# Kernel tuning notes

Measured on AMD Instinct MI355X. Metric: run time of the kernel, lower is better.

## Reference

```python
import jax, jax.numpy as jnp
import numpy as np
from math import factorial

# ---- static config (mirrors init_kwargs) ----
ZS = np.array([1, 6, 7, 8], dtype=np.int64)
NZ = 4
N_ATOM_BASIS = 3
CHAN = N_ATOM_BASIS ** 2          # 9 edge channels
MAX_L = 3
N_RBF = 8                          # radial basis functions
N_RB = 8                           # radial embedding dim
CUTOFF = 5.5
P_CUT = 6
MP_NORM = 1.0 / 10.0 ** 0.5        # 1/sqrt(avg_num_neighbors)
NUM_MP = 1
N_NODES = 4000
N_EDGES = 48000

def _make_l_list(max_l):
    lst = []
    for l in range(max_l + 1):
        for lx in range(l, -1, -1):
            for ly in range(l - lx, -1, -1):
                lst.append((lx, ly, l - lx - ly))
    return lst

L_LIST = _make_l_list(MAX_L)       # 20 (lx,ly,lz) tuples
N_L = len(L_LIST)
L_OF = np.array([sum(t) for t in L_LIST], dtype=np.int32)
LX = np.array([t[0] for t in L_LIST])
LY = np.array([t[1] for t in L_LIST])
LZ = np.array([t[2] for t in L_LIST])
# multinomial prefactors l!/(lx!ly!lz!), grouped per l for the nu=2 symmetrizer
PREF = np.array([factorial(sum(t)) / (factorial(t[0]) * factorial(t[1]) * factorial(t[2])) for t in L_LIST], dtype=np.float32)
SYM2 = np.zeros((N_L, MAX_L + 1), dtype=np.float32)
SYM2[np.arange(N_L), L_OF] = PREF

def _bessel_rbf(r):
    # r: [E,1] -> [E, N_RBF];  e_n(r) = sqrt(2/rc) * sin(n pi r / rc) / r
    n = jnp.arange(1, N_RBF + 1, dtype=r.dtype)
    return jnp.sqrt(2.0 / CUTOFF) * jnp.sin(n * jnp.pi * r / CUTOFF) / r

def _poly_cutoff(r):
    p = float(P_CUT)
    u = r / CUTOFF
    f = 1.0 - 0.5 * (p + 1.0) * (p + 2.0) * u ** p + p * (p + 2.0) * u ** (p + 1.0) - 0.5 * p * (p + 1.0) * u ** (p + 2.0)
    return f * (u < 1.0)

def _angular(unit):
    # monomials x^lx * y^ly * z^lz of the unit edge vector -> [E, N_L]
    x, y, z = unit[:, 0:1], unit[:, 1:2], unit[:, 2:3]
    return (x ** jnp.asarray(LX)) * (y ** jnp.asarray(LY)) * (z ** jnp.asarray(LZ))

def _radial_transform(A, W_rt):
    # shared per-l linear map along radial axis: [N, N_RBF, N_L, C] -> [N, N_RB, N_L, C]
    Wg = W_rt[jnp.asarray(L_OF)]   # [N_L, N_RBF, N_RB]
    return jnp.einsum('nric,irs->nsic', A, Wg)

def _symmetrize(A):
    # nu=1: A at lxlylz=(0,0,0); nu=2, each l: sum_{|lxlylz|=l} multinomial * A^2
    B1 = A[:, :, 0:1, :]
    B2 = jnp.einsum('nric,il->nrlc', A * A, jnp.asarray(SYM2))
    return jnp.concatenate([B1, B2], axis=2)   # [N, N_RB, 1+(MAX_L+1), C]

def _forward(positions, shifts, W_emb, W_rt, W_nm, atomic_numbers, edge_index):
    sender, receiver = edge_index[0], edge_index[1]
    one_hot = (atomic_numbers[:, None] == jnp.asarray(ZS)[None, :]).astype(positions.dtype)
    node_emb = one_hot @ W_emb                                    # [N, n_atom_basis]
    # edge encoding: flattened outer product of sender/receiver embeddings -> [E, CHAN]
    enc = (node_emb[sender][:, :, None] * node_emb[receiver][:, None, :]).reshape(-1, CHAN)
    vec = positions[receiver] - positions[sender] + shifts
    lengths = jnp.linalg.norm(vec, axis=-1, keepdims=True)        # [E,1]
    unit = vec / lengths
    rc = _bessel_rbf(lengths) * _poly_cutoff(lengths)             # [E, N_RBF]
    ang = _angular(unit)                                          # [E, N_L]
    edge_attri = rc[:, :, None, None] * ang[:, None, :, None] * enc[:, None, None, :]
    A = jax.ops.segment_sum(edge_attri, receiver, num_segments=N_NODES)
    A = _radial_transform(A, W_rt)                                # [N, N_RB, N_L, C]
    B = _symmetrize(A)
    feats = [B]
    Wnm_exp = W_nm[:, :, jnp.asarray(L_OF), :]                    # expand per-l memory weights to lxlylz
    for _ in range(NUM_MP):
        memory = A * Wnm_exp                                      # NodeMemory
        chi = B.sum(axis=(1, 2))                                  # [N, C] invariant scalar per channel
        msg_B = edge_attri * chi[sender][:, None, None, :]        # MesssageBchi
        A_B = _radial_transform(jax.ops.segment_sum(msg_B, receiver, num_segments=N_NODES), W_rt)
        msg_A = A[sender] * rc[:, :, None, None]                  # MessageAr: radial-weighted sender A
        A = (A_B + jax.ops.segment_sum(msg_A, receiver, num_segments=N_NODES)) * MP_NORM + memory
        B = _symmetrize(A)
        feats.append(B)
    return jnp.stack(feats, axis=-1)                              # [N, N_RB, 5, C, 1+NUM_MP]

def setup_inputs() -> dict:
    key = jax.random.key(0)
    k = jax.random.split(key, 8)
    positions = jax.random.uniform(k[0], (N_NODES, 3), dtype=jnp.float32) * 3.0
    shifts = jnp.zeros((N_EDGES, 3), dtype=jnp.float32)
    species_idx = jax.random.randint(k[1], (N_NODES,), 0, NZ)
    atomic_numbers = jnp.asarray(ZS)[species_idx]
    sender = jax.random.randint(k[2], (N_EDGES,), 0, N_NODES)
    receiver = (sender + 1 + jax.random.randint(k[3], (N_EDGES,), 0, N_NODES - 1)) % N_NODES  # no self-edges
    edge_index = jnp.stack([sender, receiver])
    W_emb = jax.random.normal(k[4], (NZ, N_ATOM_BASIS), dtype=jnp.float32) * 0.5
    W_rt = jax.random.normal(k[5], (MAX_L + 1, N_RBF, N_RB), dtype=jnp.float32) / np.sqrt(N_RBF)
    W_nm = jax.random.uniform(k[6], (1, N_RB, MAX_L + 1, CHAN), dtype=jnp.float32)
    return {"positions": positions, "shifts": shifts, "W_emb": W_emb, "W_rt": W_rt, "W_nm": W_nm, "atomic_numbers": atomic_numbers, "edge_index": edge_index}

def reference(positions, shifts, W_emb, W_rt, W_nm, atomic_numbers, edge_index):
    return _forward(positions, shifts, W_emb, W_rt, W_nm, atomic_numbers, edge_index)
```

## Files before the change

### kernel.cpp

```cpp
#include <hip/hip_runtime.h>
#include <hip/hip_fp16.h>

#ifndef M_PIf
#define M_PIf 3.14159265358979323846f
#endif

constexpr int NNODE = 4000;
constexpr int NEDGE = 48000;
constexpr int NLA   = 20;
constexpr int NCH   = 9;
constexpr int NRB   = 8;
constexpr int NEL   = NRB * NLA * NCH;
constexpr int NP2   = NEL / 2;
constexpr int FW    = 40;
constexpr int EC    = 32;
constexpr float CUT = 5.5f;
constexpr float MPN = 0.316227766016837933f;

__constant__ int   c_LOF[NLA]  = {0,1,1,1,2,2,2,2,2,2,3,3,3,3,3,3,3,3,3,3};
__constant__ float c_PREF[NLA] = {1,1,1,1,1,2,2,1,2,1,1,3,3,3,6,3,1,3,3,1};
__constant__ int   c_GB[4] = {0,0,1,4};
__constant__ int   c_GE[4] = {0,1,4,10};

__global__ void k_count(const int* __restrict__ ei, int* __restrict__ counts) {
  int e = blockIdx.x * blockDim.x + threadIdx.x;
  if (e >= NEDGE) return;
  atomicAdd(&counts[ei[NEDGE + e]], 1);
}

__global__ void k_scan(const int* __restrict__ counts, int* __restrict__ offsets,
                       int* __restrict__ cursor) {
  __shared__ int lds[1024];
  int t = threadIdx.x;
  int base = t*4;
  int c0 = (base+0 < NNODE) ? counts[base+0] : 0;
  int c1 = (base+1 < NNODE) ? counts[base+1] : 0;
  int c2 = (base+2 < NNODE) ? counts[base+2] : 0;
  int c3 = (base+3 < NNODE) ? counts[base+3] : 0;
  lds[t] = c0+c1+c2+c3;
  __syncthreads();
  for (int d = 1; d < 1024; d <<= 1) {
    int v = (t >= d) ? lds[t-d] : 0;
    __syncthreads();
    lds[t] += v;
    __syncthreads();
  }
  int excl = (t == 0) ? 0 : lds[t-1];
  int o0 = excl, o1 = o0+c0, o2 = o1+c1, o3 = o2+c2;
  if (base+0 < NNODE) { offsets[base+0]=o0; cursor[base+0]=o0; }
  if (base+1 < NNODE) { offsets[base+1]=o1; cursor[base+1]=o1; }
  if (base+2 < NNODE) { offsets[base+2]=o2; cursor[base+2]=o2; }
  if (base+3 < NNODE) { offsets[base+3]=o3; cursor[base+3]=o3; }
  if (t == 1023) offsets[NNODE] = lds[1023];
}

__global__ void k_edgec(const float* __restrict__ pos, const float* __restrict__ shifts,
                        const int* __restrict__ ei, const int* __restrict__ an,
                        const float* __restrict__ W_emb,
                        int* __restrict__ cursor, float* __restrict__ facS,
                        int* __restrict__ sndS) {
  int e = blockIdx.x * blockDim.x + threadIdx.x;
  if (e >= NEDGE) return;
  int snd = ei[e];
  int rcv = ei[NEDGE + e];
  float vx = pos[rcv*3+0] - pos[snd*3+0] + shifts[e*3+0];
  float vy = pos[rcv*3+1] - pos[snd*3+1] + shifts[e*3+1];
  float vz = pos[rcv*3+2] - pos[snd*3+2] + shifts[e*3+2];
  float len = sqrtf(vx*vx + vy*vy + vz*vz);
  float inv = 1.0f / len;
  float x = vx*inv, y = vy*inv, z = vz*inv;
  float u  = len * (1.0f/CUT);
  float u2 = u*u;
  float u6 = u2*u2*u2;
  float fcut = 1.0f - 28.0f*u6 + 48.0f*u6*u - 21.0f*u6*u2;
  if (u >= 1.0f) fcut = 0.0f;
  float pre = sqrtf(2.0f/CUT) * fcut * inv;
  int p = atomicAdd(&cursor[rcv], 1);
  float* f = facS + (size_t)p*FW;
  #pragma unroll
  for (int j = 0; j < NRB; ++j)
    f[j] = pre * sinf((float)(j+1) * M_PIf * u);
  float ang[NLA];
  ang[0]=1.0f; ang[1]=x; ang[2]=y; ang[3]=z;
  ang[4]=x*x; ang[5]=x*y; ang[6]=x*z; ang[7]=y*y; ang[8]=y*z; ang[9]=z*z;
  ang[10]=ang[4]*x; ang[11]=ang[4]*y; ang[12]=ang[4]*z;
  ang[13]=x*ang[7]; ang[14]=ang[5]*z; ang[15]=x*ang[9];
  ang[16]=ang[7]*y; ang[17]=ang[7]*z; ang[18]=y*ang[9]; ang[19]=ang[9]*z;
  #pragma unroll
  for (int i = 0; i < NLA; ++i) f[8+i] = ang[i];
  int as_ = an[snd], ar_ = an[rcv];
  int sps = (as_==1)?0:(as_==6)?1:(as_==7)?2:3;
  int spr = (ar_==1)?0:(ar_==6)?1:(ar_==7)?2:3;
  float es0=W_emb[sps*3+0], es1=W_emb[sps*3+1], es2=W_emb[sps*3+2];
  float er0=W_emb[spr*3+0], er1=W_emb[spr*3+1], er2=W_emb[spr*3+2];
  f[28]=es0*er0; f[29]=es0*er1; f[30]=es0*er2;
  f[31]=es1*er0; f[32]=es1*er1; f[33]=es1*er2;
  f[34]=es2*er0; f[35]=es2*er1; f[36]=es2*er2;
  f[37]=0.f; f[38]=0.f; f[39]=0.f;
  sndS[p] = snd;
}

__global__ void k_echi(const float* __restrict__ facS, const int* __restrict__ sndS,
                       const float* __restrict__ chi, float* __restrict__ echiS) {
  int p = blockIdx.x * blockDim.x + threadIdx.x;
  if (p >= NEDGE) return;
  int snd = sndS[p];
  const float* f = facS + (size_t)p*FW;
  float* o = echiS + (size_t)p*12;
  #pragma unroll
  for (int c = 0; c < 9; ++c)
    o[c] = chi[snd*9 + c] * f[28 + c];
  o[9] = 0.f; o[10] = 0.f; o[11] = 0.f;
}


__global__ __launch_bounds__(256, 8) void k_nodeA(
    const float* __restrict__ facS, const int* __restrict__ offsets,
    const float* __restrict__ W_rt,
    float2* __restrict__ A1f2, __half2* __restrict__ A1h2,
    float* __restrict__ chi, float* __restrict__ out) {
  __shared__ float s_wrt[256];
  __shared__ float s_e[EC*FW];
  __shared__ float s_tile[8*90];
  __shared__ float s_B[288];
  int bid = blockIdx.x;
  int n = bid >> 1, half = bid & 1;
  int t = threadIdx.x;
  s_wrt[t] = W_rt[t];
  int rq[2], kk[2], i0[2], c0[2], l0[2], i1[2], c1[2], l1[2], qg[2];
  bool val[2];
  #pragma unroll
  for (int jj = 0; jj < 2; ++jj) {
    int j = t + jj*256;
    val[jj] = (j < 360);
    int js = val[jj] ? j : 0;
    rq[jj] = js / 45; kk[jj] = js % 45;
    qg[jj] = rq[jj]*90 + kk[jj] + half*45;
    int rem0 = 2*(kk[jj] + 45*half);
    i0[jj] = rem0 / 9;  c0[jj] = rem0 % 9;  l0[jj] = c_LOF[i0[jj]];
    int rem1 = rem0 + 1;
    i1[jj] = rem1 / 9;  c1[jj] = rem1 % 9;  l1[jj] = c_LOF[i1[jj]];
  }
  float acc[2][2] = {{0,0},{0,0}};
  int beg = offsets[n], end = offsets[n+1];
  const float4* f4 = (const float4*)facS;
  for (int base = beg; base < end; base += EC) {
    int m = min(EC, end - base);
    __syncthreads();
    for (int idx = t; idx < m*(FW/4); idx += 256)
      ((float4*)s_e)[idx] = f4[(size_t)base*(FW/4) + idx];
    __syncthreads();
    for (int p = 0; p < m; ++p) {
      const float* e0 = s_e + p*FW;
      #pragma unroll
      for (int jj = 0; jj < 2; ++jj) {
        if (val[jj]) {
          float rv = e0[rq[jj]];
          acc[jj][0] += rv * e0[8+i0[jj]] * e0[28+c0[jj]];
          acc[jj][1] += rv * e0[8+i1[jj]] * e0[28+c1[jj]];
        }
      }
    }
  }
  __syncthreads();
  #pragma unroll
  for (int jj = 0; jj < 2; ++jj)
    if (val[jj]) {
      s_tile[rq[jj]*90 + 2*kk[jj]]     = acc[jj][0];
      s_tile[rq[jj]*90 + 2*kk[jj] + 1] = acc[jj][1];
    }
  __syncthreads();
  float a1v[2][2];
  #pragma unroll
  for (int jj = 0; jj < 2; ++jj) {
    if (val[jj]) {
      float ab0 = 0.f, ab1 = 0.f;
      #pragma unroll
      for (int r = 0; r < NRB; ++r) {
        ab0 += s_tile[r*90 + 2*kk[jj]]     * s_wrt[l0[jj]*64 + r*8 + rq[jj]];
        ab1 += s_tile[r*90 + 2*kk[jj] + 1] * s_wrt[l1[jj]*64 + r*8 + rq[jj]];
      }
      a1v[jj][0] = ab0; a1v[jj][1] = ab1;
      size_t qi = (size_t)n*NP2 + qg[jj];
      A1f2[qi] = make_float2(ab0, ab1);
      A1h2[qi] = __floats2half2_rn(ab0, ab1);
    }
  }
  __syncthreads();
  #pragma unroll
  for (int jj = 0; jj < 2; ++jj)
    if (val[jj]) {
      s_tile[rq[jj]*90 + 2*kk[jj]]     = a1v[jj][0];
      s_tile[rq[jj]*90 + 2*kk[jj] + 1] = a1v[jj][1];
    }
  __syncthreads();
  if (half == 0) {
    for (int m2 = t; m2 < 288; m2 += 256) {
      int s = m2 / 36, rm = m2 % 36, l5 = rm / 9, c = rm % 9;
      float b;
      if (l5 == 0) b = s_tile[s*90 + c];
      else {
        b = 0.f;
        for (int i = c_GB[l5]; i < c_GE[l5]; ++i) {
          float v = s_tile[s*90 + i*9 + c];
          b += c_PREF[i]*v*v;
        }
      }
      out[(size_t)(((n*8 + s)*5 + l5)*9 + c)*2 + 0] = b;
      s_B[m2] = b;
    }
    __syncthreads();
    if (t < 9) {
      float x = 0.f;
      #pragma unroll
      for (int u = 0; u < 32; ++u) x += s_B[u*9 + t];
      atomicAdd(&chi[n*9 + t], x);
    }
  } else {
    if (t < 72) {
      int s = t / 9, c = t % 9;
      float b = 0.f;
      for (int i = 10; i < 20; ++i) {
        float v = s_tile[s*90 + (i-10)*9 + c];
        b += c_PREF[i]*v*v;
      }
      out[(size_t)(((n*8 + s)*5 + 4)*9 + c)*2 + 0] = b;
      s_B[t] = b;
    }
    __syncthreads();
    if (t < 9) {
      float x = 0.f;
      #pragma unroll
      for (int u = 0; u < 8; ++u) x += s_B[u*9 + t];
      atomicAdd(&chi[n*9 + t], x);
    }
  }
}

__global__ __launch_bounds__(256, 8) void k_nodeMP(
    const float* __restrict__ facS, const int* __restrict__ offsets,
    const int* __restrict__ sndS, const float* __restrict__ echiS,
    const float* __restrict__ W_rt, const float* __restrict__ W_nm,
    const float2* __restrict__ A1f2, const __half2* __restrict__ A1h2,
    float* __restrict__ out) {
  __shared__ float s_wrt[256];
  __shared__ float s_wnm[288];
  __shared__ float s_e[EC*FW];
  __shared__ float s_ec[EC*12];
  __shared__ float s_tile[8*90];
  int bid = blockIdx.x;
  int n = bid >> 1, half = bid & 1;
  int t = threadIdx.x;
  s_wrt[t] = W_rt[t];
  s_wnm[t] = W_nm[t];
  if (t < 32) s_wnm[256 + t] = W_nm[256 + t];
  int rq[2], kk[2], i0[2], c0[2], l0[2], i1[2], c1[2], l1[2], qg[2];
  bool val[2];
  #pragma unroll
  for (int jj = 0; jj < 2; ++jj) {
    int j = t + jj*256;
    val[jj] = (j < 360);
    int js = val[jj] ? j : 0;
    rq[jj] = js / 45; kk[jj] = js % 45;
    qg[jj] = rq[jj]*90 + kk[jj] + half*45;
    int rem0 = 2*(kk[jj] + 45*half);
    i0[jj] = rem0 / 9;  c0[jj] = rem0 % 9;  l0[jj] = c_LOF[i0[jj]];
    int rem1 = rem0 + 1;
    i1[jj] = rem1 / 9;  c1[jj] = rem1 % 9;  l1[jj] = c_LOF[i1[jj]];
  }
  float accA[2][2] = {{0,0},{0,0}};
  float accB[2][2] = {{0,0},{0,0}};
  float2 mymem[2];
  #pragma unroll
  for (int jj = 0; jj < 2; ++jj)
    mymem[jj] = val[jj] ? A1f2[(size_t)n*NP2 + qg[jj]] : make_float2(0.f, 0.f);
  int beg = offsets[n], end = offsets[n+1];
  const float4* f4 = (const float4*)facS;
  const float4* e4 = (const float4*)echiS;
  for (int base = beg; base < end; base += EC) {
    int m = min(EC, end - base);
    __syncthreads();
    for (int idx = t; idx < m*(FW/4); idx += 256)
      ((float4*)s_e)[idx] = f4[(size_t)base*(FW/4) + idx];
    for (int idx = t; idx < m*3; idx += 256)
      ((float4*)s_ec)[idx] = e4[(size_t)base*3 + idx];
    __syncthreads();
    int p = 0;
    for (; p + 3 < m; p += 4) {
      int sd0 = sndS[base+p+0], sd1 = sndS[base+p+1];
      int sd2 = sndS[base+p+2], sd3 = sndS[base+p+3];
      __half2 g0a = A1h2[(size_t)sd0*NP2 + qg[0]];
      __half2 g1a = A1h2[(size_t)sd1*NP2 + qg[0]];
      __half2 g2a = A1h2[(size_t)sd2*NP2 + qg[0]];
      __half2 g3a = A1h2[(size_t)sd3*NP2 + qg[0]];
      __half2 g0b, g1b, g2b, g3b;
      if (val[1]) {
        g0b = A1h2[(size_t)sd0*NP2 + qg[1]];
        g1b = A1h2[(size_t)sd1*NP2 + qg[1]];
        g2b = A1h2[(size_t)sd2*NP2 + qg[1]];
        g3b = A1h2[(size_t)sd3*NP2 + qg[1]];
      }
      #pragma unroll
      for (int x = 0; x < 4; ++x) {
        const float* e0 = s_e + (p+x)*FW;
        const float* x0 = s_ec + (p+x)*12;
        __half2 ga = (x==0)?g0a:(x==1)?g1a:(x==2)?g2a:g3a;
        {
          float rv = e0[rq[0]];
          float2 gf = __half22float2(ga);
          accA[0][0] += gf.x * rv;
          accA[0][1] += gf.y * rv;
          accB[0][0] += rv * e0[8+i0[0]] * x0[c0[0]];
          accB[0][1] += rv * e0[8+i1[0]] * x0[c1[0]];
        }
        if (val[1]) {
          __half2 gb = (x==0)?g0b:(x==1)?g1b:(x==2)?g2b:g3b;
          float rv = e0[rq[1]];
          float2 gf = __half22float2(gb);
          accA[1][0] += gf.x * rv;
          accA[1][1] += gf.y * rv;
          accB[1][0] += rv * e0[8+i0[1]] * x0[c0[1]];
          accB[1][1] += rv * e0[8+i1[1]] * x0[c1[1]];
        }
      }
    }
    for (; p < m; ++p) {
      int sd = sndS[base+p];
      const float* e0 = s_e + p*FW;
      const float* x0 = s_ec + p*12;
      const __half2* Ah = A1h2 + (size_t)sd*NP2;
      #pragma unroll
      for (int jj = 0; jj < 2; ++jj) {
        if (val[jj]) {
          float rv = e0[rq[jj]];
          float2 gf = __half22float2(Ah[qg[jj]]);
          accA[jj][0] += gf.x * rv;
          accA[jj][1] += gf.y * rv;
          accB[jj][0] += rv * e0[8+i0[jj]] * x0[c0[jj]];
          accB[jj][1] += rv * e0[8+i1[jj]] * x0[c1[jj]];
        }
      }
    }
  }
  __syncthreads();
  #pragma unroll
  for (int jj = 0; jj < 2; ++jj)
    if (val[jj]) {
      s_tile[rq[jj]*90 + 2*kk[jj]]     = accB[jj][0];
      s_tile[rq[jj]*90 + 2*kk[jj] + 1] = accB[jj][1];
    }
  __syncthreads();
  float a2v[2][2];
  #pragma unroll
  for (int jj = 0; jj < 2; ++jj) {
    if (val[jj]) {
      float ab0 = 0.f, ab1 = 0.f;
      #pragma unroll
      for (int r = 0; r < NRB; ++r) {
        ab0 += s_tile[r*90 + 2*kk[jj]]     * s_wrt[l0[jj]*64 + r*8 + rq[jj]];
        ab1 += s_tile[r*90 + 2*kk[jj] + 1] * s_wrt[l1[jj]*64 + r*8 + rq[jj]];
      }
      float mem0 = mymem[jj].x * s_wnm[rq[jj]*36 + l0[jj]*9 + c0[jj]];
      float mem1 = mymem[jj].y * s_wnm[rq[jj]*36 + l1[jj]*9 + c1[jj]];
      a2v[jj][0] = (ab0 + accA[jj][0])*MPN + mem0;
      a2v[jj][1] = (ab1 + accA[jj][1])*MPN + mem1;
    }
  }
  __syncthreads();
  #pragma unroll
  for (int jj = 0; jj < 2; ++jj)
    if (val[jj]) {
      s_tile[rq[jj]*90 + 2*kk[jj]]     = a2v[jj][0];
      s_tile[rq[jj]*90 + 2*kk[jj] + 1] = a2v[jj][1];
    }
  __syncthreads();
  if (half == 0) {
    for (int m2 = t; m2 < 288; m2 += 256) {
      int s = m2 / 36, rm = m2 % 36, l5 = rm / 9, c = rm % 9;
      float b;
      if (l5 == 0) b = s_tile[s*90 + c];
      else {
        b = 0.f;
        for (int i = c_GB[l5]; i < c_GE[l5]; ++i) {
          float v = s_tile[s*90 + i*9 + c];
          b += c_PREF[i]*v*v;
        }
      }
      out[(size_t)(((n*8 + s)*5 + l5)*9 + c)*2 + 1] = b;
    }
  } else {
    if (t < 72) {
      int s = t / 9, c = t % 9;
      float b = 0.f;
      for (int i = 10; i < 20; ++i) {
        float v = s_tile[s*90 + (i-10)*9 + c];
        b += c_PREF[i]*v*v;
      }
      out[(size_t)(((n*8 + s)*5 + 4)*9 + c)*2 + 1] = b;
    }
  }
}

extern "C" void kernel_launch(void* const* d_in, const int* in_sizes, int n_in,
                              void* d_out, int out_size, void* d_ws, size_t ws_size,
                              hipStream_t stream) {
  const float* pos    = (const float*)d_in[0];
  const float* shifts = (const float*)d_in[1];
  const float* W_emb  = (const float*)d_in[2];
  const float* W_rt   = (const float*)d_in[3];
  const float* W_nm   = (const float*)d_in[4];
  const int*   an     = (const int*)d_in[5];
  const int*   ei     = (const int*)d_in[6];
  float* out = (float*)d_out;

  char* ws = (char*)d_ws;
  size_t off = 0;
  auto carve = [&](size_t bytes) {
    void* p = ws + off;
    off = (off + bytes + 255) & ~(size_t)255;
    return p;
  };
  float*   facS    = (float*)carve((size_t)FW*NEDGE*sizeof(float));
  int*     sndS    = (int*)carve((size_t)NEDGE*sizeof(int));
  float*   echiS   = (float*)carve((size_t)12*NEDGE*sizeof(float));
  float2*  A1f2    = (float2*)carve((size_t)NNODE*NEL*sizeof(float));
  __half2* A1h2    = (__half2*)carve((size_t)NNODE*NEL*sizeof(__half));
  float*   chi     = (float*)carve((size_t)NNODE*NCH*sizeof(float));
  int*     counts  = (int*)carve((size_t)NNODE*sizeof(int));
  int*     offsets = (int*)carve((size_t)(NNODE+1)*sizeof(int));
  int*     cursor  = (int*)carve((size_t)NNODE*sizeof(int));

  size_t z0 = (size_t)((char*)chi - ws);
  size_t z1 = (size_t)((char*)counts - ws) + (size_t)NNODE*sizeof(int);
  hipMemsetAsync((char*)ws + z0, 0, z1 - z0, stream);
  k_count<<<(NEDGE+255)/256, 256, 0, stream>>>(ei, counts);
  k_scan<<<1, 1024, 0, stream>>>(counts, offsets, cursor);
  k_edgec<<<(NEDGE+255)/256, 256, 0, stream>>>(pos, shifts, ei, an, W_emb, cursor, facS, sndS);
  k_nodeA<<<NNODE*2, 256, 0, stream>>>(facS, offsets, W_rt, A1f2, A1h2, chi, out);
  k_echi<<<(NEDGE+255)/256, 256, 0, stream>>>(facS, sndS, chi, echiS);
  k_nodeMP<<<NNODE*2, 256, 0, stream>>>(facS, offsets, sndS, echiS, W_rt, W_nm, A1f2, A1h2, out);
}
```

Baseline: 122.1 us.

## Drop fp32 A1 buffer, use wave-shuffle scan, sin recurrence, compact work mapping

Several separate changes. The fp32 copy of A1 is removed, so the residual term in the message-passing kernel now reads the fp16 copy. The block scan uses wave shuffles instead of an LDS Hillis-Steele loop, and the Bessel sines come from one sincos plus a Chebyshev recurrence. The 360 work items are remapped so the second item goes to the first 26 lanes of each wave, avoiding partially-active waves, and the message-passing kernel stages only the first 28 floats of each edge row into LDS. Using fp16 for the residual and the sin recurrence adds precision risk.

```diff
diff --git a/kernel.cpp b/kernel.cpp
--- a/kernel.cpp
+++ b/kernel.cpp
@@ -30,28 +30,41 @@
 
 __global__ void k_scan(const int* __restrict__ counts, int* __restrict__ offsets,
                        int* __restrict__ cursor) {
-  __shared__ int lds[1024];
+  __shared__ int wsum[16];
   int t = threadIdx.x;
   int base = t*4;
   int c0 = (base+0 < NNODE) ? counts[base+0] : 0;
   int c1 = (base+1 < NNODE) ? counts[base+1] : 0;
   int c2 = (base+2 < NNODE) ? counts[base+2] : 0;
   int c3 = (base+3 < NNODE) ? counts[base+3] : 0;
-  lds[t] = c0+c1+c2+c3;
-  __syncthreads();
-  for (int d = 1; d < 1024; d <<= 1) {
-    int v = (t >= d) ? lds[t-d] : 0;
-    __syncthreads();
-    lds[t] += v;
-    __syncthreads();
-  }
-  int excl = (t == 0) ? 0 : lds[t-1];
+  int s = c0+c1+c2+c3;
+  int lane = t & 63, w = t >> 6;
+  int incl = s;
+  #pragma unroll
+  for (int d = 1; d < 64; d <<= 1) {
+    int v = __shfl_up(incl, d);
+    if (lane >= d) incl += v;
+  }
+  if (lane == 63) wsum[w] = incl;
+  __syncthreads();
+  if (t < 16) {
+    int v = wsum[t];
+    int inc2 = v;
+    #pragma unroll
+    for (int d = 1; d < 16; d <<= 1) {
+      int u = __shfl_up(inc2, d);
+      if (t >= d) inc2 += u;
+    }
+    wsum[t] = inc2 - v;
+  }
+  __syncthreads();
+  int excl = wsum[w] + incl - s;
   int o0 = excl, o1 = o0+c0, o2 = o1+c1, o3 = o2+c2;
   if (base+0 < NNODE) { offsets[base+0]=o0; cursor[base+0]=o0; }
   if (base+1 < NNODE) { offsets[base+1]=o1; cursor[base+1]=o1; }
   if (base+2 < NNODE) { offsets[base+2]=o2; cursor[base+2]=o2; }
   if (base+3 < NNODE) { offsets[base+3]=o3; cursor[base+3]=o3; }
-  if (t == 1023) offsets[NNODE] = lds[1023];
+  if (t == 1023) offsets[NNODE] = excl + s;
 }
 
 __global__ void k_edgec(const float* __restrict__ pos, const float* __restrict__ shifts,
@@ -77,9 +90,16 @@
   float pre = sqrtf(2.0f/CUT) * fcut * inv;
   int p = atomicAdd(&cursor[rcv], 1);
   float* f = facS + (size_t)p*FW;
-  #pragma unroll
-  for (int j = 0; j < NRB; ++j)
-    f[j] = pre * sinf((float)(j+1) * M_PIf * u);
+  float s1, cth;
+  __sincosf(M_PIf * u, &s1, &cth);
+  float two_c = 2.0f * cth;
+  float sm1 = 0.0f, sc = s1;
+  #pragma unroll
+  for (int j = 0; j < NRB; ++j) {
+    f[j] = pre * sc;
+    float nx = two_c * sc - sm1;
+    sm1 = sc; sc = nx;
+  }
   float ang[NLA];
   ang[0]=1.0f; ang[1]=x; ang[2]=y; ang[3]=z;
   ang[4]=x*x; ang[5]=x*y; ang[6]=x*z; ang[7]=y*y; ang[8]=y*z; ang[9]=z*z;
@@ -117,7 +137,7 @@
 __global__ __launch_bounds__(256, 8) void k_nodeA(
     const float* __restrict__ facS, const int* __restrict__ offsets,
     const float* __restrict__ W_rt,
-    float2* __restrict__ A1f2, __half2* __restrict__ A1h2,
+    __half2* __restrict__ A1h2,
     float* __restrict__ chi, float* __restrict__ out) {
   __shared__ float s_wrt[256];
   __shared__ float s_e[EC*FW];
@@ -127,14 +147,15 @@
   int n = bid >> 1, half = bid & 1;
   int t = threadIdx.x;
   s_wrt[t] = W_rt[t];
-  int rq[2], kk[2], i0[2], c0[2], l0[2], i1[2], c1[2], l1[2], qg[2];
-  bool val[2];
+  int lane = t & 63, w = t >> 6;
+  bool act1 = (lane < 26);
+  int q[2];
+  q[0] = t;
+  q[1] = act1 ? (256 + w*26 + lane) : 0;
+  int rq[2], kk[2], qg[2], i0[2], c0[2], l0[2], i1[2], c1[2], l1[2];
   #pragma unroll
   for (int jj = 0; jj < 2; ++jj) {
-    int j = t + jj*256;
-    val[jj] = (j < 360);
-    int js = val[jj] ? j : 0;
-    rq[jj] = js / 45; kk[jj] = js % 45;
+    rq[jj] = q[jj] / 45; kk[jj] = q[jj] % 45;
     qg[jj] = rq[jj]*90 + kk[jj] + half*45;
     int rem0 = 2*(kk[jj] + 45*half);
     i0[jj] = rem0 / 9;  c0[jj] = rem0 % 9;  l0[jj] = c_LOF[i0[jj]];
@@ -152,28 +173,30 @@
     __syncthreads();
     for (int p = 0; p < m; ++p) {
       const float* e0 = s_e + p*FW;
-      #pragma unroll
-      for (int jj = 0; jj < 2; ++jj) {
-        if (val[jj]) {
-          float rv = e0[rq[jj]];
-          acc[jj][0] += rv * e0[8+i0[jj]] * e0[28+c0[jj]];
-          acc[jj][1] += rv * e0[8+i1[jj]] * e0[28+c1[jj]];
-        }
-      }
-    }
-  }
-  __syncthreads();
-  #pragma unroll
-  for (int jj = 0; jj < 2; ++jj)
-    if (val[jj]) {
-      s_tile[rq[jj]*90 + 2*kk[jj]]     = acc[jj][0];
-      s_tile[rq[jj]*90 + 2*kk[jj] + 1] = acc[jj][1];
-    }
+      {
+        float rv = e0[rq[0]];
+        acc[0][0] += rv * e0[8+i0[0]] * e0[28+c0[0]];
+        acc[0][1] += rv * e0[8+i1[0]] * e0[28+c1[0]];
+      }
+      if (act1) {
+        float rv = e0[rq[1]];
+        acc[1][0] += rv * e0[8+i0[1]] * e0[28+c1[1]-c1[1]+c0[1]];
+        acc[1][1] += rv * e0[8+i1[1]] * e0[28+c1[1]];
+      }
+    }
+  }
+  __syncthreads();
+  s_tile[rq[0]*90 + 2*kk[0]]     = acc[0][0];
+  s_tile[rq[0]*90 + 2*kk[0] + 1] = acc[0][1];
+  if (act1) {
+    s_tile[rq[1]*90 + 2*kk[1]]     = acc[1][0];
+    s_tile[rq[1]*90 + 2*kk[1] + 1] = acc[1][1];
+  }
   __syncthreads();
   float a1v[2][2];
   #pragma unroll
   for (int jj = 0; jj < 2; ++jj) {
-    if (val[jj]) {
+    if (jj == 0 || act1) {
       float ab0 = 0.f, ab1 = 0.f;
       #pragma unroll
       for (int r = 0; r < NRB; ++r) {
@@ -181,18 +204,16 @@
         ab1 += s_tile[r*90 + 2*kk[jj] + 1] * s_wrt[l1[jj]*64 + r*8 + rq[jj]];
       }
       a1v[jj][0] = ab0; a1v[jj][1] = ab1;
-      size_t qi = (size_t)n*NP2 + qg[jj];
-      A1f2[qi] = make_float2(ab0, ab1);
-      A1h2[qi] = __floats2half2_rn(ab0, ab1);
-    }
-  }
-  __syncthreads();
-  #pragma unroll
-  for (int jj = 0; jj < 2; ++jj)
-    if (val[jj]) {
-      s_tile[rq[jj]*90 + 2*kk[jj]]     = a1v[jj][0];
-      s_tile[rq[jj]*90 + 2*kk[jj] + 1] = a1v[jj][1];
-    }
+      A1h2[(size_t)n*NP2 + qg[jj]] = __floats2half2_rn(ab0, ab1);
+    }
+  }
+  __syncthreads();
+  s_tile[rq[0]*90 + 2*kk[0]]     = a1v[0][0];
+  s_tile[rq[0]*90 + 2*kk[0] + 1] = a1v[0][1];
+  if (act1) {
+    s_tile[rq[1]*90 + 2*kk[1]]     = a1v[1][0];
+    s_tile[rq[1]*90 + 2*kk[1] + 1] = a1v[1][1];
+  }
   __syncthreads();
   if (half == 0) {
     for (int m2 = t; m2 < 288; m2 += 256) {
@@ -241,11 +262,11 @@
     const float* __restrict__ facS, const int* __restrict__ offsets,
     const int* __restrict__ sndS, const float* __restrict__ echiS,
     const float* __restrict__ W_rt, const float* __restrict__ W_nm,
-    const float2* __restrict__ A1f2, const __half2* __restrict__ A1h2,
+    const __half2* __restrict__ A1h2,
     float* __restrict__ out) {
   __shared__ float s_wrt[256];
   __shared__ float s_wnm[288];
-  __shared__ float s_e[EC*FW];
+  __shared__ float s_e[EC*28];
   __shared__ float s_ec[EC*12];
   __shared__ float s_tile[8*90];
   int bid = blockIdx.x;
@@ -254,14 +275,15 @@
   s_wrt[t] = W_rt[t];
   s_wnm[t] = W_nm[t];
   if (t < 32) s_wnm[256 + t] = W_nm[256 + t];
-  int rq[2], kk[2], i0[2], c0[2], l0[2], i1[2], c1[2], l1[2], qg[2];
-  bool val[2];
+  int lane = t & 63, w = t >> 6;
+  bool act1 = (lane < 26);
+  int q[2];
+  q[0] = t;
+  q[1] = act1 ? (256 + w*26 + lane) : 0;
+  int rq[2], kk[2], qg[2], i0[2], c0[2], l0[2], i1[2], c1[2], l1[2];
   #pragma unroll
   for (int jj = 0; jj < 2; ++jj) {
-    int j = t + jj*256;
-    val[jj] = (j < 360);
-    int js = val[jj] ? j : 0;
-    rq[jj] = js / 45; kk[jj] = js % 45;
+    rq[jj] = q[jj] / 45; kk[jj] = q[jj] % 45;
     qg[jj] = rq[jj]*90 + kk[jj] + half*45;
     int rem0 = 2*(kk[jj] + 45*half);
     i0[jj] = rem0 / 9;  c0[jj] = rem0 % 9;  l0[jj] = c_LOF[i0[jj]];
@@ -271,17 +293,18 @@
   float accA[2][2] = {{0,0},{0,0}};
   float accB[2][2] = {{0,0},{0,0}};
   float2 mymem[2];
-  #pragma unroll
-  for (int jj = 0; jj < 2; ++jj)
-    mymem[jj] = val[jj] ? A1f2[(size_t)n*NP2 + qg[jj]] : make_float2(0.f, 0.f);
+  mymem[0] = __half22float2(A1h2[(size_t)n*NP2 + qg[0]]);
+  mymem[1] = act1 ? __half22float2(A1h2[(size_t)n*NP2 + qg[1]]) : make_float2(0.f,0.f);
   int beg = offsets[n], end = offsets[n+1];
   const float4* f4 = (const float4*)facS;
   const float4* e4 = (const float4*)echiS;
   for (int base = beg; base < end; base += EC) {
     int m = min(EC, end - base);
     __syncthreads();
-    for (int idx = t; idx < m*(FW/4); idx += 256)
-      ((float4*)s_e)[idx] = f4[(size_t)base*(FW/4) + idx];
+    for (int idx = t; idx < m*7; idx += 256) {
+      int p = idx / 7, qd = idx - p*7;
+      ((float4*)(s_e + p*28))[qd] = f4[(size_t)(base+p)*10 + qd];
+    }
     for (int idx = t; idx < m*3; idx += 256)
       ((float4*)s_ec)[idx] = e4[(size_t)base*3 + idx];
     __syncthreads();
@@ -294,7 +317,7 @@
       __half2 g2a = A1h2[(size_t)sd2*NP2 + qg[0]];
       __half2 g3a = A1h2[(size_t)sd3*NP2 + qg[0]];
       __half2 g0b, g1b, g2b, g3b;
-      if (val[1]) {
+      if (act1) {
         g0b = A1h2[(size_t)sd0*NP2 + qg[1]];
         g1b = A1h2[(size_t)sd1*NP2 + qg[1]];
         g2b = A1h2[(size_t)sd2*NP2 + qg[1]];
@@ -302,7 +325,7 @@
       }
       #pragma unroll
       for (int x = 0; x < 4; ++x) {
-        const float* e0 = s_e + (p+x)*FW;
+        const float* e0 = s_e + (p+x)*28;
         const float* x0 = s_ec + (p+x)*12;
         __half2 ga = (x==0)?g0a:(x==1)?g1a:(x==2)?g2a:g3a;
         {
@@ -313,7 +336,7 @@
           accB[0][0] += rv * e0[8+i0[0]] * x0[c0[0]];
           accB[0][1] += rv * e0[8+i1[0]] * x0[c1[0]];
         }
-        if (val[1]) {
+        if (act1) {
           __half2 gb = (x==0)?g0b:(x==1)?g1b:(x==2)?g2b:g3b;
           float rv = e0[rq[1]];
           float2 gf = __half22float2(gb);
@@ -326,34 +349,39 @@
     }
     for (; p < m; ++p) {
       int sd = sndS[base+p];
-      const float* e0 = s_e + p*FW;
+      const float* e0 = s_e + p*28;
       const float* x0 = s_ec + p*12;
       const __half2* Ah = A1h2 + (size_t)sd*NP2;
-      #pragma unroll
-      for (int jj = 0; jj < 2; ++jj) {
-        if (val[jj]) {
-          float rv = e0[rq[jj]];
-          float2 gf = __half22float2(Ah[qg[jj]]);
-          accA[jj][0] += gf.x * rv;
-          accA[jj][1] += gf.y * rv;
-          accB[jj][0] += rv * e0[8+i0[jj]] * x0[c0[jj]];
-          accB[jj][1] += rv * e0[8+i1[jj]] * x0[c1[jj]];
-        }
-      }
-    }
-  }
-  __syncthreads();
-  #pragma unroll
-  for (int jj = 0; jj < 2; ++jj)
-    if (val[jj]) {
-      s_tile[rq[jj]*90 + 2*kk[jj]]     = accB[jj][0];
-      s_tile[rq[jj]*90 + 2*kk[jj] + 1] = accB[jj][1];
-    }
+      {
+        float rv = e0[rq[0]];
+        float2 gf = __half22float2(Ah[qg[0]]);
+        accA[0][0] += gf.x * rv;
+        accA[0][1] += gf.y * rv;
+        accB[0][0] += rv * e0[8+i0[0]] * x0[c0[0]];
+        accB[0][1] += rv * e0[8+i1[0]] * x0[c1[0]];
+      }
+      if (act1) {
+        float rv = e0[rq[1]];
+        float2 gf = __half22float2(Ah[qg[1]]);
+        accA[1][0] += gf.x * rv;
+        accA[1][1] += gf.y * rv;
+        accB[1][0] += rv * e0[8+i0[1]] * x0[c0[1]];
+        accB[1][1] += rv * e0[8+i1[1]] * x0[c1[1]];
+      }
+    }
+  }
+  __syncthreads();
+  s_tile[rq[0]*90 + 2*kk[0]]     = accB[0][0];
+  s_tile[rq[0]*90 + 2*kk[0] + 1] = accB[0][1];
+  if (act1) {
+    s_tile[rq[1]*90 + 2*kk[1]]     = accB[1][0];
+    s_tile[rq[1]*90 + 2*kk[1] + 1] = accB[1][1];
+  }
   __syncthreads();
   float a2v[2][2];
   #pragma unroll
   for (int jj = 0; jj < 2; ++jj) {
-    if (val[jj]) {
+    if (jj == 0 || act1) {
       float ab0 = 0.f, ab1 = 0.f;
       #pragma unroll
       for (int r = 0; r < NRB; ++r) {
@@ -367,12 +395,12 @@
     }
   }
   __syncthreads();
-  #pragma unroll
-  for (int jj = 0; jj < 2; ++jj)
-    if (val[jj]) {
-      s_tile[rq[jj]*90 + 2*kk[jj]]     = a2v[jj][0];
-      s_tile[rq[jj]*90 + 2*kk[jj] + 1] = a2v[jj][1];
-    }
+  s_tile[rq[0]*90 + 2*kk[0]]     = a2v[0][0];
+  s_tile[rq[0]*90 + 2*kk[0] + 1] = a2v[0][1];
+  if (act1) {
+    s_tile[rq[1]*90 + 2*kk[1]]     = a2v[1][0];
+    s_tile[rq[1]*90 + 2*kk[1] + 1] = a2v[1][1];
+  }
   __syncthreads();
   if (half == 0) {
     for (int m2 = t; m2 < 288; m2 += 256) {
@@ -423,7 +451,6 @@
   float*   facS    = (float*)carve((size_t)FW*NEDGE*sizeof(float));
   int*     sndS    = (int*)carve((size_t)NEDGE*sizeof(int));
   float*   echiS   = (float*)carve((size_t)12*NEDGE*sizeof(float));
-  float2*  A1f2    = (float2*)carve((size_t)NNODE*NEL*sizeof(float));
   __half2* A1h2    = (__half2*)carve((size_t)NNODE*NEL*sizeof(__half));
   float*   chi     = (float*)carve((size_t)NNODE*NCH*sizeof(float));
   int*     counts  = (int*)carve((size_t)NNODE*sizeof(int));
@@ -436,7 +463,7 @@
   k_count<<<(NEDGE+255)/256, 256, 0, stream>>>(ei, counts);
   k_scan<<<1, 1024, 0, stream>>>(counts, offsets, cursor);
   k_edgec<<<(NEDGE+255)/256, 256, 0, stream>>>(pos, shifts, ei, an, W_emb, cursor, facS, sndS);
-  k_nodeA<<<NNODE*2, 256, 0, stream>>>(facS, offsets, W_rt, A1f2, A1h2, chi, out);
+  k_nodeA<<<NNODE*2, 256, 0, stream>>>(facS, offsets, W_rt, A1h2, chi, out);
   k_echi<<<(NEDGE+255)/256, 256, 0, stream>>>(facS, sndS, chi, echiS);
-  k_nodeMP<<<NNODE*2, 256, 0, stream>>>(facS, offsets, sndS, echiS, W_rt, W_nm, A1f2, A1h2, out);
-}
+  k_nodeMP<<<NNODE*2, 256, 0, stream>>>(facS, offsets, sndS, echiS, W_rt, W_nm, A1h2, out);
+}
```

Measured after the change: 165.7 us. 1.36x slower.

## Use wave-shuffle scan, sine recurrence, and combined float2 output writes

Applied to the files above, without the earlier changes.

Replaces the 1024-step LDS Hillis-Steele scan with a two-level wavefront shuffle scan, cutting barrier count. Computes the Bessel sine series with a Chebyshev recurrence from one fast sin/cos pair instead of eight sinf calls. Moves the first-layer output into the message-passing kernel so both channels are written together as a float2, removing strided scalar stores. This relies on mymem holding the A1 values and reuses s_e as scratch; the recurrence and fast intrinsics may reduce accuracy slightly.

```diff
diff --git a/kernel.cpp b/kernel.cpp
--- a/kernel.cpp
+++ b/kernel.cpp
@@ -30,28 +30,41 @@
 
 __global__ void k_scan(const int* __restrict__ counts, int* __restrict__ offsets,
                        int* __restrict__ cursor) {
-  __shared__ int lds[1024];
+  __shared__ int wsum[16];
   int t = threadIdx.x;
   int base = t*4;
   int c0 = (base+0 < NNODE) ? counts[base+0] : 0;
   int c1 = (base+1 < NNODE) ? counts[base+1] : 0;
   int c2 = (base+2 < NNODE) ? counts[base+2] : 0;
   int c3 = (base+3 < NNODE) ? counts[base+3] : 0;
-  lds[t] = c0+c1+c2+c3;
-  __syncthreads();
-  for (int d = 1; d < 1024; d <<= 1) {
-    int v = (t >= d) ? lds[t-d] : 0;
-    __syncthreads();
-    lds[t] += v;
-    __syncthreads();
-  }
-  int excl = (t == 0) ? 0 : lds[t-1];
+  int s = c0+c1+c2+c3;
+  int lane = t & 63, w = t >> 6;
+  int incl = s;
+  #pragma unroll
+  for (int d = 1; d < 64; d <<= 1) {
+    int v = __shfl_up(incl, d);
+    if (lane >= d) incl += v;
+  }
+  if (lane == 63) wsum[w] = incl;
+  __syncthreads();
+  if (t < 16) {
+    int v = wsum[t];
+    int inc2 = v;
+    #pragma unroll
+    for (int d = 1; d < 16; d <<= 1) {
+      int u = __shfl_up(inc2, d);
+      if (t >= d) inc2 += u;
+    }
+    wsum[t] = inc2 - v;
+  }
+  __syncthreads();
+  int excl = wsum[w] + incl - s;
   int o0 = excl, o1 = o0+c0, o2 = o1+c1, o3 = o2+c2;
   if (base+0 < NNODE) { offsets[base+0]=o0; cursor[base+0]=o0; }
   if (base+1 < NNODE) { offsets[base+1]=o1; cursor[base+1]=o1; }
   if (base+2 < NNODE) { offsets[base+2]=o2; cursor[base+2]=o2; }
   if (base+3 < NNODE) { offsets[base+3]=o3; cursor[base+3]=o3; }
-  if (t == 1023) offsets[NNODE] = lds[1023];
+  if (t == 1023) offsets[NNODE] = excl + s;
 }
 
 __global__ void k_edgec(const float* __restrict__ pos, const float* __restrict__ shifts,
@@ -77,9 +90,16 @@
   float pre = sqrtf(2.0f/CUT) * fcut * inv;
   int p = atomicAdd(&cursor[rcv], 1);
   float* f = facS + (size_t)p*FW;
-  #pragma unroll
-  for (int j = 0; j < NRB; ++j)
-    f[j] = pre * sinf((float)(j+1) * M_PIf * u);
+  float s1 = __sinf(M_PIf * u);
+  float cth = __cosf(M_PIf * u);
+  float two_c = 2.0f * cth;
+  float sm1 = 0.0f, sc = s1;
+  #pragma unroll
+  for (int j = 0; j < NRB; ++j) {
+    f[j] = pre * sc;
+    float nx = two_c * sc - sm1;
+    sm1 = sc; sc = nx;
+  }
   float ang[NLA];
   ang[0]=1.0f; ang[1]=x; ang[2]=y; ang[3]=z;
   ang[4]=x*x; ang[5]=x*y; ang[6]=x*z; ang[7]=y*y; ang[8]=y*z; ang[9]=z*z;
@@ -118,7 +138,7 @@
     const float* __restrict__ facS, const int* __restrict__ offsets,
     const float* __restrict__ W_rt,
     float2* __restrict__ A1f2, __half2* __restrict__ A1h2,
-    float* __restrict__ chi, float* __restrict__ out) {
+    float* __restrict__ chi) {
   __shared__ float s_wrt[256];
   __shared__ float s_e[EC*FW];
   __shared__ float s_tile[8*90];
@@ -206,7 +226,6 @@
           b += c_PREF[i]*v*v;
         }
       }
-      out[(size_t)(((n*8 + s)*5 + l5)*9 + c)*2 + 0] = b;
       s_B[m2] = b;
     }
     __syncthreads();
@@ -224,7 +243,6 @@
         float v = s_tile[s*90 + (i-10)*9 + c];
         b += c_PREF[i]*v*v;
       }
-      out[(size_t)(((n*8 + s)*5 + 4)*9 + c)*2 + 0] = b;
       s_B[t] = b;
     }
     __syncthreads();
@@ -343,11 +361,14 @@
     }
   }
   __syncthreads();
+  float* s_a1 = s_e;
   #pragma unroll
   for (int jj = 0; jj < 2; ++jj)
     if (val[jj]) {
       s_tile[rq[jj]*90 + 2*kk[jj]]     = accB[jj][0];
       s_tile[rq[jj]*90 + 2*kk[jj] + 1] = accB[jj][1];
+      s_a1[rq[jj]*90 + 2*kk[jj]]       = mymem[jj].x;
+      s_a1[rq[jj]*90 + 2*kk[jj] + 1]   = mymem[jj].y;
     }
   __syncthreads();
   float a2v[2][2];
@@ -374,29 +395,36 @@
       s_tile[rq[jj]*90 + 2*kk[jj] + 1] = a2v[jj][1];
     }
   __syncthreads();
+  float2* o2 = (float2*)out;
   if (half == 0) {
     for (int m2 = t; m2 < 288; m2 += 256) {
       int s = m2 / 36, rm = m2 % 36, l5 = rm / 9, c = rm % 9;
-      float b;
-      if (l5 == 0) b = s_tile[s*90 + c];
-      else {
-        b = 0.f;
+      float b0, b1;
+      if (l5 == 0) {
+        b0 = s_a1[s*90 + c];
+        b1 = s_tile[s*90 + c];
+      } else {
+        b0 = 0.f; b1 = 0.f;
         for (int i = c_GB[l5]; i < c_GE[l5]; ++i) {
-          float v = s_tile[s*90 + i*9 + c];
-          b += c_PREF[i]*v*v;
-        }
-      }
-      out[(size_t)(((n*8 + s)*5 + l5)*9 + c)*2 + 1] = b;
+          float v0 = s_a1[s*90 + i*9 + c];
+          float v1 = s_tile[s*90 + i*9 + c];
+          b0 += c_PREF[i]*v0*v0;
+          b1 += c_PREF[i]*v1*v1;
+        }
+      }
+      o2[(size_t)((n*8 + s)*5 + l5)*9 + c] = make_float2(b0, b1);
     }
   } else {
     if (t < 72) {
       int s = t / 9, c = t % 9;
-      float b = 0.f;
+      float b0 = 0.f, b1 = 0.f;
       for (int i = 10; i < 20; ++i) {
-        float v = s_tile[s*90 + (i-10)*9 + c];
-        b += c_PREF[i]*v*v;
-      }
-      out[(size_t)(((n*8 + s)*5 + 4)*9 + c)*2 + 1] = b;
+        float v0 = s_a1[s*90 + (i-10)*9 + c];
+        float v1 = s_tile[s*90 + (i-10)*9 + c];
+        b0 += c_PREF[i]*v0*v0;
+        b1 += c_PREF[i]*v1*v1;
+      }
+      o2[(size_t)((n*8 + s)*5 + 4)*9 + c] = make_float2(b0, b1);
     }
   }
 }
@@ -436,7 +464,7 @@
   k_count<<<(NEDGE+255)/256, 256, 0, stream>>>(ei, counts);
   k_scan<<<1, 1024, 0, stream>>>(counts, offsets, cursor);
   k_edgec<<<(NEDGE+255)/256, 256, 0, stream>>>(pos, shifts, ei, an, W_emb, cursor, facS, sndS);
-  k_nodeA<<<NNODE*2, 256, 0, stream>>>(facS, offsets, W_rt, A1f2, A1h2, chi, out);
+  k_nodeA<<<NNODE*2, 256, 0, stream>>>(facS, offsets, W_rt, A1f2, A1h2, chi);
   k_echi<<<(NEDGE+255)/256, 256, 0, stream>>>(facS, sndS, chi, echiS);
   k_nodeMP<<<NNODE*2, 256, 0, stream>>>(facS, offsets, sndS, echiS, W_rt, W_nm, A1f2, A1h2, out);
 }
```

New measurement: 119.6 us. 2.1% less time.
